# Kernel tuning notes

Hardware: AMD Instinct MI355X
Metric: run time of the kernel (lower is better)

## Reference

```python
import jax, jax.numpy as jnp
import numpy as np

EPS = 1e-7  # CIoULoss eps

def setup_inputs() -> dict:
    key = jax.random.key(0)
    k1, k2, k3, k4, k5 = jax.random.split(key, 5)
    B, A, C, H, W, T, stride = 64, 3, 11, 80, 80, 50, 8
    img = H * stride
    predictions = jax.random.normal(k1, (B, A * (5 + C), H, W), dtype=jnp.float32)
    xy1 = jax.random.uniform(k2, (B, T, 2), minval=0.0, maxval=0.75 * img)
    wh = jax.random.uniform(k3, (B, T, 2), minval=4.0, maxval=0.2 * img)
    boxes = jnp.concatenate([xy1, xy1 + wh], axis=-1)  # xyxy, all in-image
    classes = jax.random.randint(k4, (B, T), 0, C)
    anchors = jax.random.uniform(k5, (A, 2), minval=1.0, maxval=5.0)
    return {"predictions": predictions, "boxes": boxes, "classes": classes,
            "anchors": anchors, "stride": stride}

def _bce_logits(x, t):
    # BCEWithLogits, no reduction: softplus(x) - x*t
    return jnp.logaddexp(0.0, x) - x * t

def _ciou(pb, tb):
    # pb, tb: (..., 4) xyxy -> CIoU loss per box
    px1, py1, px2, py2 = pb[..., 0], pb[..., 1], pb[..., 2], pb[..., 3]
    tx1, ty1, tx2, ty2 = tb[..., 0], tb[..., 1], tb[..., 2], tb[..., 3]
    iw = jnp.clip(jnp.minimum(px2, tx2) - jnp.maximum(px1, tx1), 0.0)
    ih = jnp.clip(jnp.minimum(py2, ty2) - jnp.maximum(py1, ty1), 0.0)
    inter = iw * ih
    pa = (px2 - px1) * (py2 - py1)
    ta = (tx2 - tx1) * (ty2 - ty1)
    union = pa + ta - inter + EPS
    iou = inter / union
    cw = jnp.maximum(px2, tx2) - jnp.minimum(px1, tx1)
    ch = jnp.maximum(py2, ty2) - jnp.minimum(py1, ty1)
    c2 = cw * cw + ch * ch + EPS
    rho2 = ((px1 + px2 - tx1 - tx2) ** 2 + (py1 + py2 - ty1 - ty2) ** 2) / 4.0
    v = (4.0 / np.pi ** 2) * (jnp.arctan((tx2 - tx1) / (ty2 - ty1 + EPS))
                              - jnp.arctan((px2 - px1) / (py2 - py1 + EPS))) ** 2
    alpha = jax.lax.stop_gradient(v / (v - iou + 1.0 + EPS))
    return 1.0 - iou + rho2 / c2 + alpha * v

def reference(predictions, boxes, classes, anchors, stride):
    A = anchors.shape[0]
    B, ch, H, W = predictions.shape
    C = ch // A - 5
    obj_w, coord_w, cls_w = 1.0, 5.0, 1.0
    s = jnp.float32(stride)

    # (B, A, H, W, 5+C)
    pred = predictions.reshape(B, A, 5 + C, H, W).transpose(0, 1, 3, 4, 2)
    pred_obj = pred[..., 4]

    # targets -> grid units
    cxcy = (boxes[..., :2] + boxes[..., 2:]) * 0.5
    wh = boxes[..., 2:] - boxes[..., :2]
    gx, gy = cxcy[..., 0] / s, cxcy[..., 1] / s
    gwh = wh / s                                   # (B, T, 2)
    gw, gh = gwh[..., 0], gwh[..., 1]
    gi = gx.astype(jnp.int32)                      # int() truncation, gx >= 0
    gj = gy.astype(jnp.int32)
    valid = (gi >= 0) & (gi < W) & (gj >= 0) & (gj < H)
    gi_c = jnp.clip(gi, 0, W - 1)
    gj_c = jnp.clip(gj, 0, H - 1)

    # anchor matching: argmin over max(wh/a, a/wh) penalty
    r = gwh[..., None, :] / anchors                # (B, T, A, 2)
    penalty = jnp.maximum(r, 1.0 / r).max(-1)      # (B, T, A)
    best = jnp.argmin(penalty, axis=-1)            # (B, T)
    aw, ah = anchors[best, 0], anchors[best, 1]

    b_idx = jnp.arange(B)[:, None]
    p = pred[b_idx, best, gj_c, gi_c]              # (B, T, 5+C)

    # decoded pred box -> CIoU vs target (note: tx/ty/tw/th MSE is dead code in the original)
    px = jax.nn.sigmoid(p[..., 0]) + gi_c.astype(p.dtype)
    py = jax.nn.sigmoid(p[..., 1]) + gj_c.astype(p.dtype)
    pw = jnp.exp(p[..., 2]) * aw
    ph = jnp.exp(p[..., 3]) * ah
    pred_xyxy = jnp.stack([px - pw / 2, py - ph / 2, px + pw / 2, py + ph / 2], axis=-1) * s
    loss_box = jnp.sum(_ciou(pred_xyxy, boxes) * valid)

    onehot = jax.nn.one_hot(classes, C, dtype=p.dtype)
    loss_cls = jnp.sum(_bce_logits(p[..., 5:], onehot).sum(-1) * valid)

    # objectness: the original adds BCE(pred_obj, cumulative target mask).mean() once per
    # batch item, with obj_mask accumulated across batch items -> entry from batch k is
    # counted (B - k) times in the -x*t term.
    mask = jnp.zeros((B, A, H, W), dtype=bool).at[b_idx, best, gj_c, gi_c].max(valid)
    n_tot = B * A * H * W
    sp_mean = jnp.mean(jnp.logaddexp(0.0, pred_obj))
    w_b = (B - jnp.arange(B)).astype(pred_obj.dtype)
    masked_sum = jnp.sum(pred_obj * mask, axis=(1, 2, 3))   # (B,)
    loss_obj = B * sp_mean - jnp.sum(w_b * masked_sum) / n_tot

    num_targets = boxes.shape[0] * boxes.shape[1]  # counted before in-range check
    total = coord_w * loss_box / num_targets + obj_w * loss_obj / B + cls_w * loss_cls / num_targets
    return total
```

## Files before the change

kernel.cpp:

```cpp
#include <hip/hip_runtime.h>
#include <math.h>

#define B_   64
#define A_   3
#define C_   11
#define H_   80
#define W_   80
#define T_   50
#define CH_  (5 + C_)
#define PLANE (H_ * W_)
#define NTOT (B_ * A_ * H_ * W_)
#define EPSF 1e-7f

__device__ __forceinline__ float softplusf(float x) {
    return fmaxf(x, 0.0f) + log1pf(expf(-fabsf(x)));
}


__global__ void targets_kernel(const float* __restrict__ pred,
                               const float* __restrict__ boxes,
                               const int*   __restrict__ classes,
                               const float* __restrict__ anchors,
                               const int*   __restrict__ stride_p,
                               float*        __restrict__ acc,
                               unsigned int* __restrict__ maskbits) {
    int idx = blockIdx.x * blockDim.x + threadIdx.x;
    if (idx >= B_ * T_) return;
    int b = idx / T_;

    int iv = stride_p[0];
    float s = (iv > 0 && iv < 100000) ? (float)iv : __int_as_float(iv);

    const float* bx = boxes + (size_t)idx * 4;
    float x1 = bx[0], y1 = bx[1], x2 = bx[2], y2 = bx[3];

    float cx = (x1 + x2) * 0.5f, cy = (y1 + y2) * 0.5f;
    float tw = x2 - x1,          th = y2 - y1;
    float gx = cx / s, gy = cy / s;
    float gw = tw / s, gh = th / s;
    int gi = (int)gx, gj = (int)gy;
    if (gi < 0 || gi >= W_ || gj < 0 || gj >= H_) return;
    int gic = gi, gjc = gj;

    int best = 0; float bestp = 3.4e38f; float aw = 1.0f, ah = 1.0f;
    #pragma unroll
    for (int a = 0; a < A_; ++a) {
        float ax = anchors[2*a], ay = anchors[2*a + 1];
        float rx = gw / ax, ry = gh / ay;
        float p = fmaxf(fmaxf(rx, 1.0f / rx), fmaxf(ry, 1.0f / ry));
        if (p < bestp) { bestp = p; best = a; aw = ax; ah = ay; }
    }

    const float* pbase = pred + ((size_t)(b * (A_ * CH_) + best * CH_)) * PLANE
                              + (size_t)gjc * W_ + gic;
    float p[CH_];
    #pragma unroll
    for (int k = 0; k < CH_; ++k) p[k] = pbase[(size_t)k * PLANE];

    float px = 1.0f / (1.0f + expf(-p[0])) + (float)gic;
    float py = 1.0f / (1.0f + expf(-p[1])) + (float)gjc;
    float pw = expf(p[2]) * aw;
    float ph = expf(p[3]) * ah;
    float px1 = (px - pw * 0.5f) * s, py1 = (py - ph * 0.5f) * s;
    float px2 = (px + pw * 0.5f) * s, py2 = (py + ph * 0.5f) * s;

    float iw = fmaxf(fminf(px2, x2) - fmaxf(px1, x1), 0.0f);
    float ih = fmaxf(fminf(py2, y2) - fmaxf(py1, y1), 0.0f);
    float inter = iw * ih;
    float pa = (px2 - px1) * (py2 - py1);
    float ta = (x2 - x1) * (y2 - y1);
    float uni = pa + ta - inter + EPSF;
    float iou = inter / uni;
    float cw  = fmaxf(px2, x2) - fminf(px1, x1);
    float chh = fmaxf(py2, y2) - fminf(py1, y1);
    float c2  = cw * cw + chh * chh + EPSF;
    float dx = px1 + px2 - x1 - x2;
    float dy = py1 + py2 - y1 - y2;
    float rho2 = (dx * dx + dy * dy) * 0.25f;
    const float FOUR_OVER_PI2 = 4.0f / (float)(M_PI * M_PI);
    float dv = atanf((x2 - x1) / (y2 - y1 + EPSF)) - atanf((px2 - px1) / (py2 - py1 + EPSF));
    float v = FOUR_OVER_PI2 * dv * dv;
    float alpha = v / (v - iou + 1.0f + EPSF);
    float ciou_loss = 1.0f - iou + rho2 / c2 + alpha * v;

    int cls = classes[idx];
    float cls_sum = 0.0f;
    #pragma unroll
    for (int c = 0; c < C_; ++c) {
        float xk = p[5 + c];
        cls_sum += softplusf(xk) - ((c == cls) ? xk : 0.0f);
    }

    atomicAdd(&acc[0], ciou_loss);
    atomicAdd(&acc[1], cls_sum);

    int cell = ((b * A_ + best) * H_ + gjc) * W_ + gic;
    unsigned int word = (unsigned int)cell >> 5, bit = 1u << (cell & 31);
    unsigned int old = atomicOr(&maskbits[word], bit);
    if (!(old & bit)) {
        atomicAdd(&acc[3], (float)(B_ - b) * p[4]);
    }
}

__global__ void obj_softplus_kernel(const float* __restrict__ pred,
                                    float* __restrict__ acc) {
    int gid = blockIdx.x * blockDim.x + threadIdx.x;
    int j = gid * 4;
    float lsum = 0.0f;
    if (j < NTOT) {
        int plane = j / PLANE;
        int off   = j - plane * PLANE;
        int b = plane / A_, a = plane - b * A_;
        const float* ptr = pred + ((size_t)(b * (A_ * CH_) + a * CH_ + 4)) * PLANE + off;
        float4 v4 = *(const float4*)ptr;
        lsum = softplusf(v4.x) + softplusf(v4.y) + softplusf(v4.z) + softplusf(v4.w);
    }
    #pragma unroll
    for (int o = 32; o > 0; o >>= 1) lsum += __shfl_down(lsum, o, 64);
    __shared__ float wsum[4];
    int lane = threadIdx.x & 63, wid = threadIdx.x >> 6;
    if (lane == 0) wsum[wid] = lsum;
    __syncthreads();
    if (threadIdx.x == 0) {
        atomicAdd(&acc[2], wsum[0] + wsum[1] + wsum[2] + wsum[3]);
    }
}

__global__ void finalize_kernel(const float* __restrict__ acc, float* __restrict__ out) {
    float loss_box = acc[0], loss_cls = acc[1], sp_sum = acc[2], wsum = acc[3];
    float sp_mean  = sp_sum / (float)NTOT;
    float loss_obj = (float)B_ * sp_mean - wsum / (float)NTOT;
    float nt = (float)(B_ * T_);
    out[0] = 5.0f * loss_box / nt + loss_obj / (float)B_ + loss_cls / nt;
}

extern "C" void kernel_launch(void* const* d_in, const int* in_sizes, int n_in,
                              void* d_out, int out_size, void* d_ws, size_t ws_size,
                              hipStream_t stream) {
    const float* pred    = (const float*)d_in[0];
    const float* boxes   = (const float*)d_in[1];
    const int*   classes = (const int*)  d_in[2];
    const float* anchors = (const float*)d_in[3];
    const int*   stride  = (const int*)  d_in[4];

    float*        acc      = (float*)d_ws;
    unsigned int* maskbits = (unsigned int*)((char*)d_ws + 256);
    size_t clear_bytes = 256 + (size_t)(NTOT / 32) * 4;
    hipMemsetAsync(d_ws, 0, clear_bytes, stream);

    targets_kernel<<<(B_ * T_ + 255) / 256, 256, 0, stream>>>(
        pred, boxes, classes, anchors, stride, acc, maskbits);

    obj_softplus_kernel<<<NTOT / 4 / 256, 256, 0, stream>>>(pred, acc);

    finalize_kernel<<<1, 1, 0, stream>>>(acc, (float*)d_out);
}
```

Measured before the change: 142.9 us.

## Fuse target and objectness kernels, replace atomics and memset with deterministic dedup

Merges the per-target loss kernel and the objectness softplus kernel into one launch whose blocks are split by role, with each objectness block reducing a whole plane. Global float atomics and the bitmask memset are replaced by per-block partial sums and per-target cell indices written to workspace. The first-occurrence deduplication moves into the finalize kernel, done by a linear scan in shared memory. This saves a memset, a launch and the atomic contention, but adds a serial O(T) scan per target and keeps only 205 blocks on the large reduction.

```diff
diff --git a/kernel.cpp b/kernel.cpp
--- a/kernel.cpp
+++ b/kernel.cpp
@@ -9,129 +9,175 @@
 #define T_   50
 #define CH_  (5 + C_)
 #define PLANE (H_ * W_)
+#define NT   (B_ * T_)
 #define NTOT (B_ * A_ * H_ * W_)
+#define NPLANES (B_ * A_)
+#define NBLK_T 13
+#define NBLK   (NBLK_T + NPLANES)
 #define EPSF 1e-7f
+
+#define WS_BOX  0
+#define WS_CLS  16
+#define WS_SP   32
+#define WS_WOBJ 224
+#define WS_CELL 3424
 
 __device__ __forceinline__ float softplusf(float x) {
     return fmaxf(x, 0.0f) + log1pf(expf(-fabsf(x)));
 }
 
+template <int NTHREADS>
+__device__ __forceinline__ float block_sum(float v, float* lds) {
+    #pragma unroll
+    for (int o = 32; o > 0; o >>= 1) v += __shfl_down(v, o, 64);
+    int lane = threadIdx.x & 63, wid = threadIdx.x >> 6;
+    if (lane == 0) lds[wid] = v;
+    __syncthreads();
+    float r = 0.0f;
+    if (threadIdx.x == 0) {
+        #pragma unroll
+        for (int i = 0; i < NTHREADS / 64; ++i) r += lds[i];
+    }
+    __syncthreads();
+    return r;
+}
 
-__global__ void targets_kernel(const float* __restrict__ pred,
-                               const float* __restrict__ boxes,
-                               const int*   __restrict__ classes,
-                               const float* __restrict__ anchors,
-                               const int*   __restrict__ stride_p,
-                               float*        __restrict__ acc,
-                               unsigned int* __restrict__ maskbits) {
-    int idx = blockIdx.x * blockDim.x + threadIdx.x;
-    if (idx >= B_ * T_) return;
-    int b = idx / T_;
+__global__ __launch_bounds__(256)
+void main_kernel(const float* __restrict__ pred,
+                 const float* __restrict__ boxes,
+                 const int*   __restrict__ classes,
+                 const float* __restrict__ anchors,
+                 const int*   __restrict__ stride_p,
+                 float* __restrict__ ws) {
+    __shared__ float lds[4];
+    int blk = blockIdx.x, tid = threadIdx.x;
 
-    int iv = stride_p[0];
-    float s = (iv > 0 && iv < 100000) ? (float)iv : __int_as_float(iv);
+    if (blk < NBLK_T) {
+        int idx = blk * 256 + tid;
+        float box_l = 0.0f, cls_l = 0.0f;
+        if (idx < NT) {
+            int b = idx / T_;
+            int iv = stride_p[0];
+            float s = (iv > 0 && iv < 100000) ? (float)iv : __int_as_float(iv);
 
-    const float* bx = boxes + (size_t)idx * 4;
-    float x1 = bx[0], y1 = bx[1], x2 = bx[2], y2 = bx[3];
+            const float* bx = boxes + (size_t)idx * 4;
+            float x1 = bx[0], y1 = bx[1], x2 = bx[2], y2 = bx[3];
+            float cx = (x1 + x2) * 0.5f, cy = (y1 + y2) * 0.5f;
+            float gw = (x2 - x1) / s,    gh = (y2 - y1) / s;
+            float gx = cx / s,           gy = cy / s;
+            int gi = (int)gx, gj = (int)gy;
+            bool valid = (gi >= 0 && gi < W_ && gj >= 0 && gj < H_);
 
-    float cx = (x1 + x2) * 0.5f, cy = (y1 + y2) * 0.5f;
-    float tw = x2 - x1,          th = y2 - y1;
-    float gx = cx / s, gy = cy / s;
-    float gw = tw / s, gh = th / s;
-    int gi = (int)gx, gj = (int)gy;
-    if (gi < 0 || gi >= W_ || gj < 0 || gj >= H_) return;
-    int gic = gi, gjc = gj;
+            int cell = -1;
+            float wobj = 0.0f;
+            if (valid) {
+                int best = 0; float bestp = 3.4e38f, aw = 1.0f, ah = 1.0f;
+                #pragma unroll
+                for (int a = 0; a < A_; ++a) {
+                    float ax = anchors[2*a], ay = anchors[2*a+1];
+                    float rx = gw / ax, ry = gh / ay;
+                    float p = fmaxf(fmaxf(rx, 1.0f/rx), fmaxf(ry, 1.0f/ry));
+                    if (p < bestp) { bestp = p; best = a; aw = ax; ah = ay; }
+                }
 
-    int best = 0; float bestp = 3.4e38f; float aw = 1.0f, ah = 1.0f;
-    #pragma unroll
-    for (int a = 0; a < A_; ++a) {
-        float ax = anchors[2*a], ay = anchors[2*a + 1];
-        float rx = gw / ax, ry = gh / ay;
-        float p = fmaxf(fmaxf(rx, 1.0f / rx), fmaxf(ry, 1.0f / ry));
-        if (p < bestp) { bestp = p; best = a; aw = ax; ah = ay; }
-    }
+                const float* pbase = pred + ((size_t)(b * (A_*CH_) + best*CH_)) * PLANE
+                                          + (size_t)gj * W_ + gi;
+                float p[CH_];
+                #pragma unroll
+                for (int k = 0; k < CH_; ++k) p[k] = pbase[(size_t)k * PLANE];
 
-    const float* pbase = pred + ((size_t)(b * (A_ * CH_) + best * CH_)) * PLANE
-                              + (size_t)gjc * W_ + gic;
-    float p[CH_];
-    #pragma unroll
-    for (int k = 0; k < CH_; ++k) p[k] = pbase[(size_t)k * PLANE];
+                float px = 1.0f / (1.0f + expf(-p[0])) + (float)gi;
+                float py = 1.0f / (1.0f + expf(-p[1])) + (float)gj;
+                float pw = expf(p[2]) * aw;
+                float ph = expf(p[3]) * ah;
+                float px1 = (px - pw*0.5f)*s, py1 = (py - ph*0.5f)*s;
+                float px2 = (px + pw*0.5f)*s, py2 = (py + ph*0.5f)*s;
 
-    float px = 1.0f / (1.0f + expf(-p[0])) + (float)gic;
-    float py = 1.0f / (1.0f + expf(-p[1])) + (float)gjc;
-    float pw = expf(p[2]) * aw;
-    float ph = expf(p[3]) * ah;
-    float px1 = (px - pw * 0.5f) * s, py1 = (py - ph * 0.5f) * s;
-    float px2 = (px + pw * 0.5f) * s, py2 = (py + ph * 0.5f) * s;
+                float iw = fmaxf(fminf(px2, x2) - fmaxf(px1, x1), 0.0f);
+                float ih = fmaxf(fminf(py2, y2) - fmaxf(py1, y1), 0.0f);
+                float inter = iw * ih;
+                float pa = (px2 - px1) * (py2 - py1);
+                float ta = (x2 - x1) * (y2 - y1);
+                float uni = pa + ta - inter + EPSF;
+                float iou = inter / uni;
+                float cw  = fmaxf(px2, x2) - fminf(px1, x1);
+                float chh = fmaxf(py2, y2) - fminf(py1, y1);
+                float c2  = cw*cw + chh*chh + EPSF;
+                float dx = px1 + px2 - x1 - x2;
+                float dy = py1 + py2 - y1 - y2;
+                float rho2 = (dx*dx + dy*dy) * 0.25f;
+                const float FOUR_OVER_PI2 = 4.0f / (float)(M_PI * M_PI);
+                float dv = atanf((x2-x1)/(y2-y1+EPSF)) - atanf((px2-px1)/(py2-py1+EPSF));
+                float v = FOUR_OVER_PI2 * dv * dv;
+                float alpha = v / (v - iou + 1.0f + EPSF);
+                box_l = 1.0f - iou + rho2 / c2 + alpha * v;
 
-    float iw = fmaxf(fminf(px2, x2) - fmaxf(px1, x1), 0.0f);
-    float ih = fmaxf(fminf(py2, y2) - fmaxf(py1, y1), 0.0f);
-    float inter = iw * ih;
-    float pa = (px2 - px1) * (py2 - py1);
-    float ta = (x2 - x1) * (y2 - y1);
-    float uni = pa + ta - inter + EPSF;
-    float iou = inter / uni;
-    float cw  = fmaxf(px2, x2) - fminf(px1, x1);
-    float chh = fmaxf(py2, y2) - fminf(py1, y1);
-    float c2  = cw * cw + chh * chh + EPSF;
-    float dx = px1 + px2 - x1 - x2;
-    float dy = py1 + py2 - y1 - y2;
-    float rho2 = (dx * dx + dy * dy) * 0.25f;
-    const float FOUR_OVER_PI2 = 4.0f / (float)(M_PI * M_PI);
-    float dv = atanf((x2 - x1) / (y2 - y1 + EPSF)) - atanf((px2 - px1) / (py2 - py1 + EPSF));
-    float v = FOUR_OVER_PI2 * dv * dv;
-    float alpha = v / (v - iou + 1.0f + EPSF);
-    float ciou_loss = 1.0f - iou + rho2 / c2 + alpha * v;
+                int cls = classes[idx];
+                #pragma unroll
+                for (int c = 0; c < C_; ++c) {
+                    float xk = p[5 + c];
+                    cls_l += softplusf(xk) - ((c == cls) ? xk : 0.0f);
+                }
 
-    int cls = classes[idx];
-    float cls_sum = 0.0f;
-    #pragma unroll
-    for (int c = 0; c < C_; ++c) {
-        float xk = p[5 + c];
-        cls_sum += softplusf(xk) - ((c == cls) ? xk : 0.0f);
-    }
-
-    atomicAdd(&acc[0], ciou_loss);
-    atomicAdd(&acc[1], cls_sum);
-
-    int cell = ((b * A_ + best) * H_ + gjc) * W_ + gic;
-    unsigned int word = (unsigned int)cell >> 5, bit = 1u << (cell & 31);
-    unsigned int old = atomicOr(&maskbits[word], bit);
-    if (!(old & bit)) {
-        atomicAdd(&acc[3], (float)(B_ - b) * p[4]);
+                cell = (best * H_ + gj) * W_ + gi;
+                wobj = (float)(B_ - b) * p[4];
+            }
+            ws[WS_WOBJ + idx] = wobj;
+            ((int*)ws)[WS_CELL + idx] = cell;
+        }
+        float bsum = block_sum<256>(box_l, lds);
+        float csum = block_sum<256>(cls_l, lds);
+        if (tid == 0) { ws[WS_BOX + blk] = bsum; ws[WS_CLS + blk] = csum; }
+    } else {
+        int g = blk - NBLK_T;
+        int b = g / A_, a = g - b * A_;
+        const float* ptr = pred + ((size_t)(b * (A_*CH_) + a*CH_ + 4)) * PLANE;
+        float lsum = 0.0f;
+        for (int j = tid; j < PLANE / 4; j += 256) {
+            float4 v4 = ((const float4*)ptr)[j];
+            lsum += softplusf(v4.x) + softplusf(v4.y) + softplusf(v4.z) + softplusf(v4.w);
+        }
+        float ssum = block_sum<256>(lsum, lds);
+        if (tid == 0) ws[WS_SP + g] = ssum;
     }
 }
 
-__global__ void obj_softplus_kernel(const float* __restrict__ pred,
-                                    float* __restrict__ acc) {
-    int gid = blockIdx.x * blockDim.x + threadIdx.x;
-    int j = gid * 4;
-    float lsum = 0.0f;
-    if (j < NTOT) {
-        int plane = j / PLANE;
-        int off   = j - plane * PLANE;
-        int b = plane / A_, a = plane - b * A_;
-        const float* ptr = pred + ((size_t)(b * (A_ * CH_) + a * CH_ + 4)) * PLANE + off;
-        float4 v4 = *(const float4*)ptr;
-        lsum = softplusf(v4.x) + softplusf(v4.y) + softplusf(v4.z) + softplusf(v4.w);
+__global__ __launch_bounds__(1024)
+void finalize_kernel(const float* __restrict__ ws, float* __restrict__ out) {
+    __shared__ int   s_cell[NT];
+    __shared__ float lds[16];
+    int tid = threadIdx.x;
+
+    for (int t = tid; t < NT; t += 1024) s_cell[t] = ((const int*)ws)[WS_CELL + t];
+    __syncthreads();
+
+    float w_l = 0.0f;
+    for (int t = tid; t < NT; t += 1024) {
+        int c = s_cell[t];
+        if (c >= 0) {
+            int start = (t / T_) * T_;
+            bool first = true;
+            for (int tp = start; tp < t; ++tp)
+                if (s_cell[tp] == c) { first = false; break; }
+            if (first) w_l += ws[WS_WOBJ + t];
+        }
     }
-    #pragma unroll
-    for (int o = 32; o > 0; o >>= 1) lsum += __shfl_down(lsum, o, 64);
-    __shared__ float wsum[4];
-    int lane = threadIdx.x & 63, wid = threadIdx.x >> 6;
-    if (lane == 0) wsum[wid] = lsum;
-    __syncthreads();
-    if (threadIdx.x == 0) {
-        atomicAdd(&acc[2], wsum[0] + wsum[1] + wsum[2] + wsum[3]);
+
+    float box_l = (tid < NBLK_T)   ? ws[WS_BOX + tid] : 0.0f;
+    float cls_l = (tid < NBLK_T)   ? ws[WS_CLS + tid] : 0.0f;
+    float sp_l  = (tid < NPLANES)  ? ws[WS_SP + tid]  : 0.0f;
+
+    float wsum = block_sum<1024>(w_l, lds);
+    float bsum = block_sum<1024>(box_l, lds);
+    float csum = block_sum<1024>(cls_l, lds);
+    float ssum = block_sum<1024>(sp_l, lds);
+
+    if (tid == 0) {
+        float sp_mean  = ssum / (float)NTOT;
+        float loss_obj = (float)B_ * sp_mean - wsum / (float)NTOT;
+        float nt = (float)NT;
+        out[0] = 5.0f * bsum / nt + loss_obj / (float)B_ + csum / nt;
     }
-}
-
-__global__ void finalize_kernel(const float* __restrict__ acc, float* __restrict__ out) {
-    float loss_box = acc[0], loss_cls = acc[1], sp_sum = acc[2], wsum = acc[3];
-    float sp_mean  = sp_sum / (float)NTOT;
-    float loss_obj = (float)B_ * sp_mean - wsum / (float)NTOT;
-    float nt = (float)(B_ * T_);
-    out[0] = 5.0f * loss_box / nt + loss_obj / (float)B_ + loss_cls / nt;
 }
 
 extern "C" void kernel_launch(void* const* d_in, const int* in_sizes, int n_in,
@@ -142,16 +188,8 @@
     const int*   classes = (const int*)  d_in[2];
     const float* anchors = (const float*)d_in[3];
     const int*   stride  = (const int*)  d_in[4];
+    float* ws = (float*)d_ws;
 
-    float*        acc      = (float*)d_ws;
-    unsigned int* maskbits = (unsigned int*)((char*)d_ws + 256);
-    size_t clear_bytes = 256 + (size_t)(NTOT / 32) * 4;
-    hipMemsetAsync(d_ws, 0, clear_bytes, stream);
-
-    targets_kernel<<<(B_ * T_ + 255) / 256, 256, 0, stream>>>(
-        pred, boxes, classes, anchors, stride, acc, maskbits);
-
-    obj_softplus_kernel<<<NTOT / 4 / 256, 256, 0, stream>>>(pred, acc);
-
-    finalize_kernel<<<1, 1, 0, stream>>>(acc, (float*)d_out);
+    main_kernel<<<NBLK, 256, 0, stream>>>(pred, boxes, classes, anchors, stride, ws);
+    finalize_kernel<<<1, 1024, 0, stream>>>(ws, (float*)d_out);
 }
```

Result: no change. 140.6 us (-1.7%).
